# Optimization experiments

Measured on AMD Instinct MI355X. Metric: run time of the kernel, lower is better.

Reference implementation:

```python
import jax, jax.numpy as jnp
import numpy as np

B, C, H, W = 4, 512, 48, 48
BN_EPS = 1e-5


def setup_inputs() -> dict:
    key = jax.random.key(0)
    ks = jax.random.split(key, 12)
    s = 1.0 / np.sqrt(C)  # conv2d default init scale for 1x1 kernels
    return {
        "x": jax.random.normal(ks[0], (B, C, H, W), dtype=jnp.float32),
        "from_depth_estimation": jax.random.normal(ks[1], (B, C, H, W), dtype=jnp.float32),
        "w_rgb": jax.random.uniform(ks[2], (C, C), jnp.float32, -s, s),
        "b_rgb": jax.random.uniform(ks[3], (C,), jnp.float32, -s, s),
        "w_lhs": jax.random.uniform(ks[4], (C, C), jnp.float32, -s, s),
        "b_lhs": jax.random.uniform(ks[5], (C,), jnp.float32, -s, s),
        "w_rhs": jax.random.uniform(ks[6], (C, C), jnp.float32, -s, s),
        "b_rhs": jax.random.uniform(ks[7], (C,), jnp.float32, -s, s),
        "w_dec": jax.random.uniform(ks[8], (C, C), jnp.float32, -s, s),
        "b_dec": jax.random.uniform(ks[9], (C,), jnp.float32, -s, s),
        "gamma": jnp.ones((C,), jnp.float32),
        "beta": jnp.zeros((C,), jnp.float32),
    }


def _to_tokens(t):
    # (B,C,H,W) -> (B*H*W, C)
    return t.transpose(0, 2, 3, 1).reshape(-1, t.shape[1])


def reference(x, from_depth_estimation, w_rgb, b_rgb, w_lhs, b_lhs, w_rhs, b_rhs,
              w_dec, b_dec, gamma, beta):
    # 1x1 convs == per-token linear layers; weight layout (out, in)
    xt = _to_tokens(x) @ w_rgb.T + b_rgb          # (N, C)
    dt = _to_tokens(from_depth_estimation)
    lhs = dt @ w_lhs.T + b_lhs                     # (N, C)
    rhs = dt @ w_rhs.T + b_rhs                     # (N, C)

    # global, unscaled attention over all B*H*W tokens (batch dims mixed)
    logits = lhs @ rhs.T                           # (N, N)
    weight = jax.nn.softmax(logits, axis=1)
    enhanced = weight @ xt                         # (N, C)

    enhanced = enhanced.reshape(B, H, W, C).transpose(0, 3, 1, 2)  # (B,C,H,W)

    # decoder: 1x1 conv -> BatchNorm2d (batch stats, training mode) -> ReLU
    y = jnp.einsum('bchw,oc->bohw', enhanced, w_dec) + b_dec[None, :, None, None]
    mean = y.mean(axis=(0, 2, 3), keepdims=True)
    var = y.var(axis=(0, 2, 3), keepdims=True)     # biased variance (torch BN fwd)
    y = (y - mean) * jax.lax.rsqrt(var + BN_EPS)
    y = y * gamma[None, :, None, None] + beta[None, :, None, None]
    return jax.nn.relu(y)
```

## Files before the change

kernel.cpp:

```cpp
#include <hip/hip_runtime.h>
#include <math.h>

#define Bd 4
#define Cd 512
#define Hd 48
#define Wd 48
#define HWd (Hd * Wd)
#define Nd (Bd * HWd)
#define BN_EPS 1e-5f

#define QBLK 64
#define KBLK 128
#define NKS 4
#define KSLEN (Nd / NKS)
#define AITERS (KSLEN / KBLK)

typedef _Float16 half8 __attribute__((ext_vector_type(8)));
typedef _Float16 h4 __attribute__((ext_vector_type(4)));
typedef float f32x16 __attribute__((ext_vector_type(16)));

__device__ inline void gload_lds16(const void* g, void* l) {
    __builtin_amdgcn_global_load_lds((const __attribute__((address_space(1))) void*)g,
                                     (__attribute__((address_space(3))) void*)l, 16, 0, 0);
}

__device__ inline size_t wp_idx(int o, int c) {
    return (((size_t)(o >> 5) * 32 + (c >> 4)) * 64 + ((o & 31) + 32 * ((c >> 3) & 1))) * 8 + (c & 7);
}
__device__ inline size_t qp_idx(int q, int c) {
    return (((size_t)(q >> 5) * 64 + (c >> 3)) * 32 + (q & 31)) * 8 + (c & 7);
}
__device__ inline size_t kp_idx(int n, int o) {
    return ((((size_t)(n >> 7) * 4 + ((n >> 5) & 3)) * 32 + (o >> 4)) * 64
            + ((n & 31) + 32 * ((o >> 3) & 1))) * 8 + (o & 7);
}
__device__ inline size_t vp_idx(int n, int o) {
    return ((((size_t)(n >> 7) * 16 + (o >> 5)) * 8 + ((n >> 4) & 7)) * 64
            + ((o & 31) + 32 * ((n >> 3) & 1))) * 8 + (n & 7);
}

__global__ __launch_bounds__(256) void wpack_k(const float* __restrict__ w0,
                                               const float* __restrict__ w1,
                                               const float* __restrict__ w2,
                                               const float* __restrict__ w3,
                                               _Float16* __restrict__ p0,
                                               _Float16* __restrict__ p1,
                                               _Float16* __restrict__ p2,
                                               _Float16* __restrict__ p3) {
    const float* w; _Float16* p;
    switch (blockIdx.y) {
        case 0: w = w0; p = p0; break;
        case 1: w = w1; p = p1; break;
        case 2: w = w2; p = p2; break;
        default: w = w3; p = p3; break;
    }
    int idx = blockIdx.x * 256 + threadIdx.x;
    int o = idx >> 6;
    int cc = (idx & 63) * 8;
    float4 a = *(const float4*)(w + (size_t)o * 512 + cc);
    float4 b = *(const float4*)(w + (size_t)o * 512 + cc + 4);
    half8 v = {(_Float16)a.x, (_Float16)a.y, (_Float16)a.z, (_Float16)a.w,
               (_Float16)b.x, (_Float16)b.y, (_Float16)b.z, (_Float16)b.w};
    *(half8*)(p + wp_idx(o, cc)) = v;
}

template<int INM, int OUTM>
__global__ __launch_bounds__(256, 2) void linproj_k(const void* __restrict__ in,
                                                    const _Float16* __restrict__ Wp,
                                                    const float* __restrict__ bias,
                                                    void* __restrict__ outp) {
    constexpr bool SWAP = (OUTM == 2);
    __shared__ _Float16 Xs[16384];

    const int tid = threadIdx.x;
    const int wave = tid >> 6;
    const int lane = tid & 63;
    const int l31 = lane & 31;
    const int hi32 = lane >> 5;
    const int n0 = blockIdx.x * 32;
    const int by = blockIdx.y;
    const int b = n0 / HWd;
    const int hw0 = n0 % HWd;

    {
        const int t = tid & 31;
        const int c0 = tid >> 5;
        #pragma unroll 8
        for (int k = 0; k < 64; ++k) {
            int c = c0 + 8 * k;
            float val;
            if (INM == 0)
                val = ((const float*)in)[(size_t)(b * Cd + c) * HWd + hw0 + t];
            else
                val = (float)((const _Float16*)in)[(size_t)c * Nd + n0 + t];
            if (!SWAP)
                Xs[(c >> 3) * 256 + t * 8 + (c & 7)] = (_Float16)val;
            else
                Xs[(c >> 4) * 512 + (t + 32 * ((c >> 3) & 1)) * 8 + (c & 7)] = (_Float16)val;
        }
    }
    __syncthreads();

    #pragma unroll
    for (int ot = 0; ot < 2; ++ot) {
        const int otb = by * 256 + ot * 128 + wave * 32;

        half8 wa[32];
        const _Float16* wpb = Wp + ((size_t)(otb >> 5) * 32) * 512;
        #pragma unroll
        for (int f = 0; f < 32; ++f)
            wa[f] = *(const half8*)(wpb + (size_t)f * 512 + lane * 8);

        f32x16 acc;
        #pragma unroll
        for (int r = 0; r < 16; ++r) acc[r] = 0.f;

        __builtin_amdgcn_s_setprio(1);
        #pragma unroll
        for (int f = 0; f < 32; ++f) {
            if (!SWAP) {
                half8 xb = *(const half8*)(Xs + (2 * f + hi32) * 256 + l31 * 8);
                acc = __builtin_amdgcn_mfma_f32_32x32x16_f16(wa[f], xb, acc, 0, 0, 0);
            } else {
                half8 xa = *(const half8*)(Xs + f * 512 + lane * 8);
                acc = __builtin_amdgcn_mfma_f32_32x32x16_f16(xa, wa[f], acc, 0, 0, 0);
            }
        }
        __builtin_amdgcn_s_setprio(0);

        if (OUTM == 0) {
            _Float16* Qp = (_Float16*)outp;
            #pragma unroll
            for (int q8 = 0; q8 < 4; ++q8) {
                int o = otb + 8 * q8 + 4 * hi32;
                float4 bv = *(const float4*)(bias + o);
                h4 v = {(_Float16)(acc[4 * q8 + 0] + bv.x), (_Float16)(acc[4 * q8 + 1] + bv.y),
                        (_Float16)(acc[4 * q8 + 2] + bv.z), (_Float16)(acc[4 * q8 + 3] + bv.w)};
                *(h4*)(Qp + qp_idx(n0 + l31, o)) = v;
            }
        } else if (OUTM == 1) {
            _Float16* Kp = (_Float16*)outp;
            #pragma unroll
            for (int q8 = 0; q8 < 4; ++q8) {
                int o = otb + 8 * q8 + 4 * hi32;
                float4 bv = *(const float4*)(bias + o);
                h4 v = {(_Float16)(acc[4 * q8 + 0] + bv.x), (_Float16)(acc[4 * q8 + 1] + bv.y),
                        (_Float16)(acc[4 * q8 + 2] + bv.z), (_Float16)(acc[4 * q8 + 3] + bv.w)};
                *(h4*)(Kp + kp_idx(n0 + l31, o)) = v;
            }
        } else if (OUTM == 2) {
            _Float16* Vp = (_Float16*)outp;
            int o = otb + l31;
            float bc = bias[o];
            #pragma unroll
            for (int q8 = 0; q8 < 4; ++q8) {
                int n = n0 + 8 * q8 + 4 * hi32;
                h4 v = {(_Float16)(acc[4 * q8 + 0] + bc), (_Float16)(acc[4 * q8 + 1] + bc),
                        (_Float16)(acc[4 * q8 + 2] + bc), (_Float16)(acc[4 * q8 + 3] + bc)};
                *(h4*)(Vp + vp_idx(n, o)) = v;
            }
        } else {
            float* of = (float*)outp;
            #pragma unroll
            for (int r = 0; r < 16; ++r) {
                int o = otb + (r & 3) + 8 * (r >> 2) + 4 * hi32;
                of[(size_t)(b * Cd + o) * HWd + hw0 + l31] = acc[r] + bias[o];
            }
        }
    }
}

__global__ __launch_bounds__(512, 2) void attn_v6_k(
    const _Float16* __restrict__ Qp,
    const _Float16* __restrict__ Kp,
    const _Float16* __restrict__ Vp,
    _Float16* __restrict__ partH,
    float* __restrict__ marr,
    float* __restrict__ larr) {
    __shared__ _Float16 Qs[2 * 16384];
    __shared__ _Float16 Pl[8192];
    __shared__ float tm_s[4][64], ls_s[4][64];

    const int tid = threadIdx.x;
    const int wave = tid >> 6;
    const int lane = tid & 63;
    const int l31 = lane & 31;
    const int hi32 = lane >> 5;
    const int kt = wave & 3;
    const int qg = wave >> 2;
    const int nqb = Nd / QBLK;
    const int qb = blockIdx.x % nqb;
    const int ks = blockIdx.x / nqb;
    const int q0 = qb * QBLK;
    const int kbt0 = ks * AITERS;

    {
        const _Float16* Qt = Qp + (size_t)(q0 >> 5) * 16384;
        #pragma unroll
        for (int j = 0; j < 8; ++j)
            gload_lds16(Qt + (size_t)j * 4096 + tid * 8,
                        (char*)Qs + j * 8192 + wave * 1024);
    }
    __syncthreads();

    f32x16 o_acc[2][2];
    #pragma unroll
    for (int c = 0; c < 2; ++c)
        #pragma unroll
        for (int q = 0; q < 2; ++q)
            #pragma unroll
            for (int r = 0; r < 16; ++r) o_acc[c][q][r] = 0.f;
    float m0 = -INFINITY, m1 = -INFINITY, l0 = 0.f, l1 = 0.f;

    for (int it = 0; it < AITERS; ++it) {
        const _Float16* kp = Kp + ((size_t)(kbt0 + it) * 4 + kt) * 32 * 512;
        half8 ka[32];
        #pragma unroll
        for (int f = 0; f < 32; ++f)
            ka[f] = *(const half8*)(kp + (size_t)f * 512 + lane * 8);

        f32x16 s;
        #pragma unroll
        for (int r = 0; r < 16; ++r) s[r] = 0.f;
        const _Float16* qsb = Qs + qg * 16384;
        __builtin_amdgcn_s_setprio(1);
        #pragma unroll
        for (int f = 0; f < 32; ++f) {
            half8 qb8 = *(const half8*)(qsb + (2 * f + hi32) * 256 + l31 * 8);
            s = __builtin_amdgcn_mfma_f32_32x32x16_f16(ka[f], qb8, s, 0, 0, 0);
        }
        __builtin_amdgcn_s_setprio(0);

        float tmax = s[0];
        #pragma unroll
        for (int r = 1; r < 16; ++r) tmax = fmaxf(tmax, s[r]);
        tmax = fmaxf(tmax, __shfl_xor(tmax, 32));
        if (lane < 32) tm_s[kt][qg * 32 + lane] = tmax;
        __syncthreads();

        float mn0 = fmaxf(fmaxf(fmaxf(tm_s[0][l31], tm_s[1][l31]),
                                fmaxf(tm_s[2][l31], tm_s[3][l31])), m0);
        float mn1 = fmaxf(fmaxf(fmaxf(tm_s[0][32 + l31], tm_s[1][32 + l31]),
                                fmaxf(tm_s[2][32 + l31], tm_s[3][32 + l31])), m1);
        float corr0 = __expf(m0 - mn0);
        float corr1 = __expf(m1 - mn1);
        float mn_own = qg ? mn1 : mn0;

        float p[16];
        float psum = 0.f;
        #pragma unroll
        for (int r = 0; r < 16; ++r) { p[r] = __expf(s[r] - mn_own); psum += p[r]; }
        #pragma unroll
        for (int g = 0; g < 4; ++g) {
            h4 v = {(_Float16)p[4 * g + 0], (_Float16)p[4 * g + 1],
                    (_Float16)p[4 * g + 2], (_Float16)p[4 * g + 3]};
            *(h4*)(Pl + (qg * 8 + kt * 2 + (g >> 1)) * 512 + (g & 1) * 256
                      + l31 * 8 + 4 * hi32) = v;
        }
        psum += __shfl_xor(psum, 32);
        if (lane < 32) ls_s[kt][qg * 32 + lane] = psum;
        __syncthreads();

        l0 = l0 * corr0 + (ls_s[0][l31] + ls_s[1][l31]) + (ls_s[2][l31] + ls_s[3][l31]);
        l1 = l1 * corr1 + (ls_s[0][32 + l31] + ls_s[1][32 + l31])
                        + (ls_s[2][32 + l31] + ls_s[3][32 + l31]);
        m0 = mn0; m1 = mn1;

        half8 va[16];
        #pragma unroll
        for (int cht = 0; cht < 2; ++cht)
            #pragma unroll
            for (int kc = 0; kc < 8; ++kc)
                va[cht * 8 + kc] = *(const half8*)(
                    Vp + (((size_t)(kbt0 + it) * 16 + wave * 2 + cht) * 8 + kc) * 512
                       + lane * 8);

        #pragma unroll
        for (int cht = 0; cht < 2; ++cht)
            #pragma unroll
            for (int r = 0; r < 16; ++r) {
                o_acc[cht][0][r] *= corr0;
                o_acc[cht][1][r] *= corr1;
            }

        __builtin_amdgcn_s_setprio(1);
        #pragma unroll
        for (int qt = 0; qt < 2; ++qt)
            #pragma unroll
            for (int kc = 0; kc < 8; ++kc) {
                half8 pfrag = *(const half8*)(Pl + (qt * 8 + kc) * 512
                                                 + hi32 * 256 + l31 * 8);
                #pragma unroll
                for (int cht = 0; cht < 2; ++cht)
                    o_acc[cht][qt] = __builtin_amdgcn_mfma_f32_32x32x16_f16(
                        va[cht * 8 + kc], pfrag, o_acc[cht][qt], 0, 0, 0);
            }
        __builtin_amdgcn_s_setprio(0);
    }

    float li0 = 1.f / l0, li1 = 1.f / l1;
    #pragma unroll
    for (int cht = 0; cht < 2; ++cht)
        #pragma unroll
        for (int qt = 0; qt < 2; ++qt)
            #pragma unroll
            for (int r = 0; r < 16; ++r) {
                int row = (r & 3) + 8 * (r >> 2) + 4 * hi32;
                int ch = wave * 64 + cht * 32 + row;
                int q = q0 + qt * 32 + l31;
                partH[((size_t)ks * Cd + ch) * Nd + q] =
                    (_Float16)(o_acc[cht][qt][r] * (qt ? li1 : li0));
            }
    if (wave == 0 && lane < 32) {
        marr[(size_t)ks * Nd + q0 + lane] = m0;
        larr[(size_t)ks * Nd + q0 + lane] = l0;
        marr[(size_t)ks * Nd + q0 + 32 + lane] = m1;
        larr[(size_t)ks * Nd + q0 + 32 + lane] = l1;
    }
}

__global__ __launch_bounds__(256) void merge4_k(_Float16* __restrict__ partH,
                                                const float* __restrict__ marr,
                                                const float* __restrict__ larr) {
    size_t idx = (size_t)blockIdx.x * 256 + threadIdx.x;
    if (idx >= (size_t)Cd * Nd) return;
    int q = (int)(idx % Nd);
    float mv[NKS], wv[NKS];
    float mm = -INFINITY;
    #pragma unroll
    for (int s = 0; s < NKS; ++s) { mv[s] = marr[(size_t)s * Nd + q]; mm = fmaxf(mm, mv[s]); }
    float L = 0.f;
    #pragma unroll
    for (int s = 0; s < NKS; ++s) {
        wv[s] = larr[(size_t)s * Nd + q] * __expf(mv[s] - mm);
        L += wv[s];
    }
    float val = 0.f;
    #pragma unroll
    for (int s = 0; s < NKS; ++s)
        val += wv[s] * (float)partH[(size_t)s * Cd * Nd + idx];
    partH[idx] = (_Float16)(val / L);
}

__global__ __launch_bounds__(256) void bnstats_k(const float* __restrict__ y,
                                                 const float* __restrict__ gamma,
                                                 const float* __restrict__ beta,
                                                 float* __restrict__ stats) {
    const int c = blockIdx.x;
    const int tid = threadIdx.x;
    double s = 0.0, sq = 0.0;
    for (int b = 0; b < Bd; ++b) {
        const float* p = y + (size_t)(b * Cd + c) * HWd;
        for (int i = tid; i < HWd; i += 256) {
            double v = (double)p[i];
            s += v;
            sq += v * v;
        }
    }
    #pragma unroll
    for (int off = 32; off; off >>= 1) {
        s  += __shfl_xor(s, off, 64);
        sq += __shfl_xor(sq, off, 64);
    }
    __shared__ double ss[4], sqs[4];
    int wid = tid >> 6;
    if ((tid & 63) == 0) { ss[wid] = s; sqs[wid] = sq; }
    __syncthreads();
    if (tid == 0) {
        double S = ss[0] + ss[1] + ss[2] + ss[3];
        double Q = sqs[0] + sqs[1] + sqs[2] + sqs[3];
        double mean = S / (double)Nd;
        double var = Q / (double)Nd - mean * mean;
        float inv = (float)(1.0 / sqrt(var + (double)BN_EPS));
        float sc = gamma[c] * inv;
        stats[c] = sc;
        stats[Cd + c] = beta[c] - (float)mean * sc;
    }
}

__global__ __launch_bounds__(256) void bnapply_k(float* __restrict__ y,
                                                 const float* __restrict__ stats) {
    int idx = blockIdx.x * 256 + threadIdx.x;
    if (idx >= Bd * Cd * HWd) return;
    int c = (idx / HWd) % Cd;
    float v = fmaf(y[idx], stats[c], stats[Cd + c]);
    y[idx] = fmaxf(v, 0.f);
}

extern "C" void kernel_launch(void* const* d_in, const int* in_sizes, int n_in,
                              void* d_out, int out_size, void* d_ws, size_t ws_size,
                              hipStream_t stream) {
    const float* x     = (const float*)d_in[0];
    const float* depth = (const float*)d_in[1];
    const float* w_rgb = (const float*)d_in[2];
    const float* b_rgb = (const float*)d_in[3];
    const float* w_lhs = (const float*)d_in[4];
    const float* b_lhs = (const float*)d_in[5];
    const float* w_rhs = (const float*)d_in[6];
    const float* b_rhs = (const float*)d_in[7];
    const float* w_dec = (const float*)d_in[8];
    const float* b_dec = (const float*)d_in[9];
    const float* gamma = (const float*)d_in[10];
    const float* beta  = (const float*)d_in[11];
    float* out = (float*)d_out;

    char* wsb = (char*)d_ws;
    const size_t NC = (size_t)Nd * Cd;
    _Float16* Qp    = (_Float16*)wsb;
    _Float16* Kp    = (_Float16*)(wsb + NC * 2);
    _Float16* Vp    = (_Float16*)(wsb + NC * 4);
    _Float16* partH = (_Float16*)(wsb + NC * 6);
    float* marr  = (float*)(wsb + NC * 6 + NKS * NC * 2);
    float* larr  = marr + (size_t)NKS * Nd;
    float* stats = larr + (size_t)NKS * Nd;
    _Float16* wpLhs = (_Float16*)(stats + 2 * Cd);
    _Float16* wpRhs = wpLhs + (size_t)Cd * Cd;
    _Float16* wpRgb = wpRhs + (size_t)Cd * Cd;
    _Float16* wpDec = wpRgb + (size_t)Cd * Cd;

    wpack_k<<<dim3(128, 4), 256, 0, stream>>>(w_lhs, w_rhs, w_rgb, w_dec,
                                              wpLhs, wpRhs, wpRgb, wpDec);

    dim3 gLin(Nd / 32, 2);
    linproj_k<0, 0><<<gLin, 256, 0, stream>>>(depth, wpLhs, b_lhs, Qp);
    linproj_k<0, 1><<<gLin, 256, 0, stream>>>(depth, wpRhs, b_rhs, Kp);
    linproj_k<0, 2><<<gLin, 256, 0, stream>>>(x, wpRgb, b_rgb, Vp);

    attn_v6_k<<<(Nd / QBLK) * NKS, 512, 0, stream>>>(Qp, Kp, Vp, partH, marr, larr);

    merge4_k<<<(int)((NC + 255) / 256), 256, 0, stream>>>(partH, marr, larr);

    linproj_k<3, 3><<<gLin, 256, 0, stream>>>(partH, wpDec, b_dec, out);

    bnstats_k<<<Cd, 256, 0, stream>>>(out, gamma, beta, stats);
    bnapply_k<<<(Bd * Cd * HWd + 255) / 256, 256, 0, stream>>>(out, stats);
}
```

Baseline: 371.1 us.

## Use per-wave local softmax max with lazy rescale and one barrier per tile

Each wave now exponentiates scores against its own tile-local max, so the cross-wave max exchange and one of the two barriers per iteration go away. P and the max/sum stats are double-buffered so a single barrier is enough. The running max is raised lazily: the accumulator is rescaled only when some lane's max grows, and each key sub-tile's PV product is scaled by its own factor before being added. K fragments are also loaded inline instead of being prefetched into 32 registers. In exchange, extra FMA work is added per PV MFMA pair, and the K loads are less overlapped with the MFMAs.

```diff
diff --git a/kernel.cpp b/kernel.cpp
--- a/kernel.cpp
+++ b/kernel.cpp
@@ -170,7 +170,7 @@
     }
 }
 
-__global__ __launch_bounds__(512, 2) void attn_v6_k(
+__global__ __launch_bounds__(512, 2) void attn_v8_k(
     const _Float16* __restrict__ Qp,
     const _Float16* __restrict__ Kp,
     const _Float16* __restrict__ Vp,
@@ -178,8 +178,8 @@
     float* __restrict__ marr,
     float* __restrict__ larr) {
     __shared__ _Float16 Qs[2 * 16384];
-    __shared__ _Float16 Pl[8192];
-    __shared__ float tm_s[4][64], ls_s[4][64];
+    __shared__ _Float16 Pl[2][8192];
+    __shared__ float tm_s[2][4][64], ls_s[2][4][64];
 
     const int tid = threadIdx.x;
     const int wave = tid >> 6;
@@ -210,24 +210,22 @@
         for (int q = 0; q < 2; ++q)
             #pragma unroll
             for (int r = 0; r < 16; ++r) o_acc[c][q][r] = 0.f;
-    float m0 = -INFINITY, m1 = -INFINITY, l0 = 0.f, l1 = 0.f;
+    float M0 = -INFINITY, M1 = -INFINITY, L0 = 0.f, L1 = 0.f;
 
     for (int it = 0; it < AITERS; ++it) {
+        const int bsel = it & 1;
+
         const _Float16* kp = Kp + ((size_t)(kbt0 + it) * 4 + kt) * 32 * 512;
-        half8 ka[32];
-        #pragma unroll
-        for (int f = 0; f < 32; ++f)
-            ka[f] = *(const half8*)(kp + (size_t)f * 512 + lane * 8);
-
+        const _Float16* qsb = Qs + qg * 16384;
         f32x16 s;
         #pragma unroll
         for (int r = 0; r < 16; ++r) s[r] = 0.f;
-        const _Float16* qsb = Qs + qg * 16384;
         __builtin_amdgcn_s_setprio(1);
         #pragma unroll
         for (int f = 0; f < 32; ++f) {
+            half8 ka = *(const half8*)(kp + (size_t)f * 512 + lane * 8);
             half8 qb8 = *(const half8*)(qsb + (2 * f + hi32) * 256 + l31 * 8);
-            s = __builtin_amdgcn_mfma_f32_32x32x16_f16(ka[f], qb8, s, 0, 0, 0);
+            s = __builtin_amdgcn_mfma_f32_32x32x16_f16(ka, qb8, s, 0, 0, 0);
         }
         __builtin_amdgcn_s_setprio(0);
 
@@ -235,70 +233,84 @@
         #pragma unroll
         for (int r = 1; r < 16; ++r) tmax = fmaxf(tmax, s[r]);
         tmax = fmaxf(tmax, __shfl_xor(tmax, 32));
-        if (lane < 32) tm_s[kt][qg * 32 + lane] = tmax;
-        __syncthreads();
-
-        float mn0 = fmaxf(fmaxf(fmaxf(tm_s[0][l31], tm_s[1][l31]),
-                                fmaxf(tm_s[2][l31], tm_s[3][l31])), m0);
-        float mn1 = fmaxf(fmaxf(fmaxf(tm_s[0][32 + l31], tm_s[1][32 + l31]),
-                                fmaxf(tm_s[2][32 + l31], tm_s[3][32 + l31])), m1);
-        float corr0 = __expf(m0 - mn0);
-        float corr1 = __expf(m1 - mn1);
-        float mn_own = qg ? mn1 : mn0;
 
         float p[16];
         float psum = 0.f;
         #pragma unroll
-        for (int r = 0; r < 16; ++r) { p[r] = __expf(s[r] - mn_own); psum += p[r]; }
+        for (int r = 0; r < 16; ++r) { p[r] = __expf(s[r] - tmax); psum += p[r]; }
+        psum += __shfl_xor(psum, 32);
+
         #pragma unroll
         for (int g = 0; g < 4; ++g) {
             h4 v = {(_Float16)p[4 * g + 0], (_Float16)p[4 * g + 1],
                     (_Float16)p[4 * g + 2], (_Float16)p[4 * g + 3]};
-            *(h4*)(Pl + (qg * 8 + kt * 2 + (g >> 1)) * 512 + (g & 1) * 256
+            *(h4*)(&Pl[bsel][0] + (qg * 8 + kt * 2 + (g >> 1)) * 512 + (g & 1) * 256
                       + l31 * 8 + 4 * hi32) = v;
         }
-        psum += __shfl_xor(psum, 32);
-        if (lane < 32) ls_s[kt][qg * 32 + lane] = psum;
+        if (lane < 32) {
+            tm_s[bsel][kt][qg * 32 + lane] = tmax;
+            ls_s[bsel][kt][qg * 32 + lane] = psum;
+        }
+
         __syncthreads();
 
-        l0 = l0 * corr0 + (ls_s[0][l31] + ls_s[1][l31]) + (ls_s[2][l31] + ls_s[3][l31]);
-        l1 = l1 * corr1 + (ls_s[0][32 + l31] + ls_s[1][32 + l31])
-                        + (ls_s[2][32 + l31] + ls_s[3][32 + l31]);
-        m0 = mn0; m1 = mn1;
-
-        half8 va[16];
-        #pragma unroll
-        for (int cht = 0; cht < 2; ++cht)
-            #pragma unroll
-            for (int kc = 0; kc < 8; ++kc)
-                va[cht * 8 + kc] = *(const half8*)(
-                    Vp + (((size_t)(kbt0 + it) * 16 + wave * 2 + cht) * 8 + kc) * 512
-                       + lane * 8);
-
-        #pragma unroll
-        for (int cht = 0; cht < 2; ++cht)
-            #pragma unroll
-            for (int r = 0; r < 16; ++r) {
-                o_acc[cht][0][r] *= corr0;
-                o_acc[cht][1][r] *= corr1;
-            }
-
-        __builtin_amdgcn_s_setprio(1);
-        #pragma unroll
-        for (int qt = 0; qt < 2; ++qt)
-            #pragma unroll
-            for (int kc = 0; kc < 8; ++kc) {
-                half8 pfrag = *(const half8*)(Pl + (qt * 8 + kc) * 512
-                                                 + hi32 * 256 + l31 * 8);
+        #pragma unroll
+        for (int kc2 = 0; kc2 < 4; ++kc2) {
+            float m_t0 = tm_s[bsel][kc2][l31];
+            float m_t1 = tm_s[bsel][kc2][32 + l31];
+            float ls0 = ls_s[bsel][kc2][l31];
+            float ls1 = ls_s[bsel][kc2][32 + l31];
+
+            if (!__all(m_t0 <= M0 && m_t1 <= M1)) {
+                float Mn0 = fmaxf(M0, m_t0);
+                float Mn1 = fmaxf(M1, m_t1);
+                float c0 = __expf(M0 - Mn0);
+                float c1 = __expf(M1 - Mn1);
                 #pragma unroll
                 for (int cht = 0; cht < 2; ++cht)
-                    o_acc[cht][qt] = __builtin_amdgcn_mfma_f32_32x32x16_f16(
-                        va[cht * 8 + kc], pfrag, o_acc[cht][qt], 0, 0, 0);
-            }
-        __builtin_amdgcn_s_setprio(0);
-    }
-
-    float li0 = 1.f / l0, li1 = 1.f / l1;
+                    #pragma unroll
+                    for (int r = 0; r < 16; ++r) {
+                        o_acc[cht][0][r] *= c0;
+                        o_acc[cht][1][r] *= c1;
+                    }
+                L0 *= c0; L1 *= c1;
+                M0 = Mn0; M1 = Mn1;
+            }
+            float f0 = __expf(m_t0 - M0);
+            float f1 = __expf(m_t1 - M1);
+            L0 = fmaf(ls0, f0, L0);
+            L1 = fmaf(ls1, f1, L1);
+
+            #pragma unroll
+            for (int qt = 0; qt < 2; ++qt) {
+                const _Float16* pb = &Pl[bsel][0] + (qt * 8 + kc2 * 2) * 512
+                                   + hi32 * 256 + l31 * 8;
+                half8 pf0 = *(const half8*)(pb);
+                half8 pf1 = *(const half8*)(pb + 512);
+                float fq = qt ? f1 : f0;
+                #pragma unroll
+                for (int cht = 0; cht < 2; ++cht) {
+                    const _Float16* vb = Vp
+                        + (((size_t)(kbt0 + it) * 16 + wave * 2 + cht) * 8 + kc2 * 2) * 512
+                        + lane * 8;
+                    half8 va0 = *(const half8*)(vb);
+                    half8 va1 = *(const half8*)(vb + 512);
+                    f32x16 acc;
+                    #pragma unroll
+                    for (int r = 0; r < 16; ++r) acc[r] = 0.f;
+                    __builtin_amdgcn_s_setprio(1);
+                    acc = __builtin_amdgcn_mfma_f32_32x32x16_f16(va0, pf0, acc, 0, 0, 0);
+                    acc = __builtin_amdgcn_mfma_f32_32x32x16_f16(va1, pf1, acc, 0, 0, 0);
+                    __builtin_amdgcn_s_setprio(0);
+                    #pragma unroll
+                    for (int r = 0; r < 16; ++r)
+                        o_acc[cht][qt][r] = fmaf(acc[r], fq, o_acc[cht][qt][r]);
+                }
+            }
+        }
+    }
+
+    float li0 = 1.f / L0, li1 = 1.f / L1;
     #pragma unroll
     for (int cht = 0; cht < 2; ++cht)
         #pragma unroll
@@ -312,10 +324,10 @@
                     (_Float16)(o_acc[cht][qt][r] * (qt ? li1 : li0));
             }
     if (wave == 0 && lane < 32) {
-        marr[(size_t)ks * Nd + q0 + lane] = m0;
-        larr[(size_t)ks * Nd + q0 + lane] = l0;
-        marr[(size_t)ks * Nd + q0 + 32 + lane] = m1;
-        larr[(size_t)ks * Nd + q0 + 32 + lane] = l1;
+        marr[(size_t)ks * Nd + q0 + lane] = M0;
+        larr[(size_t)ks * Nd + q0 + lane] = L0;
+        marr[(size_t)ks * Nd + q0 + 32 + lane] = M1;
+        larr[(size_t)ks * Nd + q0 + 32 + lane] = L1;
     }
 }
 
@@ -426,7 +438,7 @@
     linproj_k<0, 1><<<gLin, 256, 0, stream>>>(depth, wpRhs, b_rhs, Kp);
     linproj_k<0, 2><<<gLin, 256, 0, stream>>>(x, wpRgb, b_rgb, Vp);
 
-    attn_v6_k<<<(Nd / QBLK) * NKS, 512, 0, stream>>>(Qp, Kp, Vp, partH, marr, larr);
+    attn_v8_k<<<(Nd / QBLK) * NKS, 512, 0, stream>>>(Qp, Kp, Vp, partH, marr, larr);
 
     merge4_k<<<(int)((NC + 255) / 256), 256, 0, stream>>>(partH, marr, larr);
 
```

Result: slower. 514.0 us (+38.5%).

## Software-pipeline QK^T of next key block with PV of current block

Applied to the files above, without the earlier changes.

Restructures the attention loop so the QK^T MFMA chain for the next key block is issued right after the V loads and before the PV MFMAs of the current block. The softmax of block i can then overlap with the score computation for block i+1, hiding latency across the barriers. K fragments are now loaded inline instead of into a 32-register array, which cuts register pressure but may expose load latency. An extra 16-float accumulator stays live across the PV phase, which could strain the 2-blocks-per-CU register budget.

```diff
diff --git a/kernel.cpp b/kernel.cpp
--- a/kernel.cpp
+++ b/kernel.cpp
@@ -170,7 +170,7 @@
     }
 }
 
-__global__ __launch_bounds__(512, 2) void attn_v6_k(
+__global__ __launch_bounds__(512, 2) void attn_v12_k(
     const _Float16* __restrict__ Qp,
     const _Float16* __restrict__ Kp,
     const _Float16* __restrict__ Vp,
@@ -203,6 +203,8 @@
     }
     __syncthreads();
 
+    const _Float16* qsb = Qs + qg * 16384;
+
     f32x16 o_acc[2][2];
     #pragma unroll
     for (int c = 0; c < 2; ++c)
@@ -212,28 +214,23 @@
             for (int r = 0; r < 16; ++r) o_acc[c][q][r] = 0.f;
     float m0 = -INFINITY, m1 = -INFINITY, l0 = 0.f, l1 = 0.f;
 
+    f32x16 s_cur;
+    #pragma unroll
+    for (int r = 0; r < 16; ++r) s_cur[r] = 0.f;
+    {
+        const _Float16* kp = Kp + ((size_t)kbt0 * 4 + kt) * 32 * 512;
+        #pragma unroll
+        for (int f = 0; f < 32; ++f) {
+            half8 ka = *(const half8*)(kp + (size_t)f * 512 + lane * 8);
+            half8 qb8 = *(const half8*)(qsb + (2 * f + hi32) * 256 + l31 * 8);
+            s_cur = __builtin_amdgcn_mfma_f32_32x32x16_f16(ka, qb8, s_cur, 0, 0, 0);
+        }
+    }
+
     for (int it = 0; it < AITERS; ++it) {
-        const _Float16* kp = Kp + ((size_t)(kbt0 + it) * 4 + kt) * 32 * 512;
-        half8 ka[32];
-        #pragma unroll
-        for (int f = 0; f < 32; ++f)
-            ka[f] = *(const half8*)(kp + (size_t)f * 512 + lane * 8);
-
-        f32x16 s;
-        #pragma unroll
-        for (int r = 0; r < 16; ++r) s[r] = 0.f;
-        const _Float16* qsb = Qs + qg * 16384;
-        __builtin_amdgcn_s_setprio(1);
-        #pragma unroll
-        for (int f = 0; f < 32; ++f) {
-            half8 qb8 = *(const half8*)(qsb + (2 * f + hi32) * 256 + l31 * 8);
-            s = __builtin_amdgcn_mfma_f32_32x32x16_f16(ka[f], qb8, s, 0, 0, 0);
-        }
-        __builtin_amdgcn_s_setprio(0);
-
-        float tmax = s[0];
-        #pragma unroll
-        for (int r = 1; r < 16; ++r) tmax = fmaxf(tmax, s[r]);
+        float tmax = s_cur[0];
+        #pragma unroll
+        for (int r = 1; r < 16; ++r) tmax = fmaxf(tmax, s_cur[r]);
         tmax = fmaxf(tmax, __shfl_xor(tmax, 32));
         if (lane < 32) tm_s[kt][qg * 32 + lane] = tmax;
         __syncthreads();
@@ -249,7 +246,7 @@
         float p[16];
         float psum = 0.f;
         #pragma unroll
-        for (int r = 0; r < 16; ++r) { p[r] = __expf(s[r] - mn_own); psum += p[r]; }
+        for (int r = 0; r < 16; ++r) { p[r] = __expf(s_cur[r] - mn_own); psum += p[r]; }
         #pragma unroll
         for (int g = 0; g < 4; ++g) {
             h4 v = {(_Float16)p[4 * g + 0], (_Float16)p[4 * g + 1],
@@ -274,6 +271,21 @@
                 va[cht * 8 + kc] = *(const half8*)(
                     Vp + (((size_t)(kbt0 + it) * 16 + wave * 2 + cht) * 8 + kc) * 512
                        + lane * 8);
+
+        f32x16 s_next;
+        #pragma unroll
+        for (int r = 0; r < 16; ++r) s_next[r] = 0.f;
+        if (it + 1 < AITERS) {
+            const _Float16* kp = Kp + ((size_t)(kbt0 + it + 1) * 4 + kt) * 32 * 512;
+            __builtin_amdgcn_s_setprio(1);
+            #pragma unroll
+            for (int f = 0; f < 32; ++f) {
+                half8 ka = *(const half8*)(kp + (size_t)f * 512 + lane * 8);
+                half8 qb8 = *(const half8*)(qsb + (2 * f + hi32) * 256 + l31 * 8);
+                s_next = __builtin_amdgcn_mfma_f32_32x32x16_f16(ka, qb8, s_next, 0, 0, 0);
+            }
+            __builtin_amdgcn_s_setprio(0);
+        }
 
         #pragma unroll
         for (int cht = 0; cht < 2; ++cht)
@@ -296,6 +308,8 @@
                         va[cht * 8 + kc], pfrag, o_acc[cht][qt], 0, 0, 0);
             }
         __builtin_amdgcn_s_setprio(0);
+
+        s_cur = s_next;
     }
 
     float li0 = 1.f / l0, li1 = 1.f / l1;
@@ -410,7 +424,7 @@
     _Float16* Kp    = (_Float16*)(wsb + NC * 2);
     _Float16* Vp    = (_Float16*)(wsb + NC * 4);
     _Float16* partH = (_Float16*)(wsb + NC * 6);
-    float* marr  = (float*)(wsb + NC * 6 + NKS * NC * 2);
+    float* marr  = (float*)(wsb + NC * 6 + (size_t)NKS * NC * 2);
     float* larr  = marr + (size_t)NKS * Nd;
     float* stats = larr + (size_t)NKS * Nd;
     _Float16* wpLhs = (_Float16*)(stats + 2 * Cd);
@@ -426,7 +440,7 @@
     linproj_k<0, 1><<<gLin, 256, 0, stream>>>(depth, wpRhs, b_rhs, Kp);
     linproj_k<0, 2><<<gLin, 256, 0, stream>>>(x, wpRgb, b_rgb, Vp);
 
-    attn_v6_k<<<(Nd / QBLK) * NKS, 512, 0, stream>>>(Qp, Kp, Vp, partH, marr, larr);
+    attn_v12_k<<<(Nd / QBLK) * NKS, 512, 0, stream>>>(Qp, Kp, Vp, partH, marr, larr);
 
     merge4_k<<<(int)((NC + 255) / 256), 256, 0, stream>>>(partH, marr, larr);
 
```

Result: slower. 469.0 us (+26.4%).
